# Kernel tuning notes

Measured on AMD Instinct MI355X. Metric: run time of the kernel, lower is better.

The kernel has to match this reference:

```python
import jax, jax.numpy as jnp
import numpy as np
from jax import lax

B, C_IN, T = 1024, 9, 2048
RT = T // 4            # reduced timesteps after two MaxPool(2)
HID, OUT = 128, 64
N_NODES = B * RT


def _chain_edges(rt, batch):
    """Bidirectional chain graph per sample, offset per batch element (PyG fallback)."""
    i = np.arange(rt - 1)
    src = np.concatenate([i, i + 1])   # edge_index[0] = source j
    dst = np.concatenate([i + 1, i])   # edge_index[1] = target i
    off = (np.arange(batch) * rt)[:, None]
    src = (src[None, :] + off).reshape(-1)
    dst = (dst[None, :] + off).reshape(-1)
    # degree with self-loops (GCNConv adds self-loops): endpoints 2, interior 3
    deg = np.full(rt, 3.0, np.float32)
    deg[0] = deg[-1] = 2.0
    deg = np.tile(deg, batch)
    return jnp.asarray(src, jnp.int32), jnp.asarray(dst, jnp.int32), jnp.asarray(deg ** -0.5)


def _conv1d(x, w, b):
    # x: [B, Cin, T], w: [Cout, Cin, 5] -> [B, Cout, T] (padding=2)
    y = lax.conv_general_dilated(x, w, window_strides=(1,), padding=[(2, 2)],
                                 dimension_numbers=('NCH', 'OIH', 'NCH'))
    return y + b[None, :, None]


def _maxpool2(x):
    b, c, t = x.shape
    return x.reshape(b, c, t // 2, 2).max(axis=-1)


def _gcn(x, W, b, src, dst, dinv):
    # GCNConv: x' = D^-1/2 (A+I) D^-1/2 (x W) + b
    h = x @ W                                        # [N, F]
    norm_e = (dinv[src] * dinv[dst])[:, None]        # per-edge sym norm
    agg = jax.ops.segment_sum(h[src] * norm_e, dst, num_segments=h.shape[0])
    return agg + h * (dinv * dinv)[:, None] + b      # self-loop term: 1/deg


def setup_inputs() -> dict:
    key = jax.random.key(0)
    ks = jax.random.split(key, 12)
    s = lambda k, shp, sc: jax.random.normal(k, shp, jnp.float32) * sc
    return {
        'x': jax.random.normal(ks[0], (B, C_IN, T), jnp.float32),
        'conv1_w': s(ks[1], (16, C_IN, 5), 0.15), 'conv1_b': jnp.zeros((16,), jnp.float32),
        'conv2_w': s(ks[2], (32, 16, 5), 0.1),   'conv2_b': jnp.zeros((32,), jnp.float32),
        'gcn1_w': s(ks[3], (32, HID), 0.17),     'gcn1_b': jnp.zeros((HID,), jnp.float32),
        'gcn2_w': s(ks[4], (HID, HID), 0.09),    'gcn2_b': jnp.zeros((HID,), jnp.float32),
        'fc_w': s(ks[5], (HID, OUT), 0.09),      'fc_b': jnp.zeros((OUT,), jnp.float32),
    }


def reference(x, conv1_w, conv1_b, conv2_w, conv2_b,
              gcn1_w, gcn1_b, gcn2_w, gcn2_b, fc_w, fc_b):
    b, c, t = x.shape
    h = _maxpool2(jax.nn.relu(_conv1d(x, conv1_w, conv1_b)))   # [B,16,T/2]
    h = _maxpool2(jax.nn.relu(_conv1d(h, conv2_w, conv2_b)))   # [B,32,T/4]
    rt = h.shape[-1]
    h = jnp.transpose(h, (0, 2, 1)).reshape(b * rt, 32)        # [N,32]
    src, dst, dinv = _chain_edges(rt, b)
    h = jax.nn.relu(_gcn(h, gcn1_w, gcn1_b, src, dst, dinv))
    h = jax.nn.relu(_gcn(h, gcn2_w, gcn2_b, src, dst, dinv))
    h = h.reshape(b, rt, -1).mean(axis=1)                      # [B,HID]
    return h @ fc_w + fc_b                                     # [B,OUT]
```

## Files before the change

### kernel.cpp

```cpp
#include <hip/hip_runtime.h>
#include <hip/hip_bf16.h>

#define B_      1024
#define CIN     9
#define T0_     2048
#define C1_     16
#define C2_     32
#define RT_     512
#define NNODES  (B_ * RT_)
#define HID_    128
#define OUTF_   64

typedef __attribute__((ext_vector_type(8))) __bf16 bf16x8;
typedef __attribute__((ext_vector_type(4))) float f32x4;
typedef __attribute__((ext_vector_type(8))) unsigned short us8;

__device__ __forceinline__ float bf2f(unsigned short u) {
    union { unsigned int i; float f; } c; c.i = ((unsigned int)u) << 16; return c.f;
}
__device__ __forceinline__ unsigned short f2bf1(float f) {
    union { float f; unsigned int i; } c; c.f = f;
    return (unsigned short)((c.i + 0x8000u) >> 16);
}
__device__ __forceinline__ unsigned int f2bf2(float lo, float hi) {
    union { float f; unsigned int i; } a, b; a.f = lo; b.f = hi;
    return __builtin_amdgcn_perm(b.i + 0x8000u, a.i + 0x8000u, 0x07060302u);
}
__device__ __forceinline__ float dinv_of(int r) {
    return (r == 0 || r == RT_ - 1) ? 0.70710678118f : 0.57735026919f;
}

__global__ __launch_bounds__(256) void repack_w(
    const float* __restrict__ W1g, const float* __restrict__ W2g,
    const float* __restrict__ Wc1g, const float* __restrict__ Wc2g,
    unsigned short* __restrict__ Wb1, unsigned short* __restrict__ Wb2,
    unsigned short* __restrict__ Wc1, unsigned short* __restrict__ Wc2)
{
    const int tid = threadIdx.x;
    const int bid = blockIdx.x;
    if (bid < 8) {
        for (int i = tid; i < 512; i += 256) {
            int s = bid * 512 + i;
            int k = s >> 7, f = s & 127;
            int lane = ((k >> 3) << 4) + (f & 15);
            int e = (((f >> 4) * 64) + lane) * 8 + (k & 7);
            Wb1[e] = f2bf1(W1g[s]);
        }
    } else if (bid < 24) {
        for (int i = tid; i < 1024; i += 256) {
            int s = (bid - 8) * 1024 + i;
            int k = s >> 7, f = s & 127;
            int ks = k >> 5, lane = (((k >> 3) & 3) << 4) + (f & 15);
            int e = ((ks * 8 + (f >> 4)) * 64 + lane) * 8 + (k & 7);
            Wb2[e] = f2bf1(W2g[s]);
        }
    } else if (bid < 28) {
        for (int i = tid; i < 384; i += 256) {
            int e = (bid - 24) * 384 + i;
            int j = e & 7, lane = (e >> 3) & 63, ks = e >> 9;
            int kk = ks * 32 + (lane >> 4) * 8 + j;
            int k = kk >> 4, ci = kk & 15, co = lane & 15;
            Wc1[e] = (k < 5 && ci < CIN) ? f2bf1(Wc1g[(co * CIN + ci) * 5 + k]) : 0;
        }
    } else {
        for (int i = tid; i < 768; i += 256) {
            int e = (bid - 28) * 768 + i;
            int j = e & 7, lane = (e >> 3) & 63, nt = (e >> 9) & 1, ks = e >> 10;
            int kk = ks * 32 + (lane >> 4) * 8 + j;
            int k = kk >> 4, ci = kk & 15, co = nt * 16 + (lane & 15);
            Wc2[e] = (k < 5) ? f2bf1(Wc2g[(co * C1_ + ci) * 5 + k]) : 0;
        }
    }
}

__global__ __launch_bounds__(256, 4) void mega(
    const float* __restrict__ x,
    const unsigned short* __restrict__ Wc1,
    const unsigned short* __restrict__ Wc2,
    const unsigned short* __restrict__ Wb1,
    const unsigned short* __restrict__ Wb2,
    const float* __restrict__ c1b, const float* __restrict__ c2b,
    const float* __restrict__ g1b, const float* __restrict__ g2b,
    float* __restrict__ partials)
{
    __shared__ __align__(16) unsigned char lds[40032];
    unsigned short* xs    = (unsigned short*)(lds);
    unsigned short* y1ext = (unsigned short*)(lds + 26496);
    unsigned short* y2loc = (unsigned short*)(lds);
    unsigned short* As1   = (unsigned short*)(lds + 10560);
    unsigned short* Hq    = (unsigned short*)(lds + 22080);
    unsigned short* A2q   = (unsigned short*)(lds + 31328);

    const int tid = threadIdx.x;
    const int b = blockIdx.x >> 2;
    const int r0 = (blockIdx.x & 3) * 128;

    const int lane = tid & 63, wave = tid >> 6;
    const int m = lane & 15, q = lane >> 4;
    const int ft0 = wave * 2;

    bf16x8 wfB[3];
    #pragma unroll
    for (int ks = 0; ks < 3; ks++) wfB[ks] = *(const bf16x8*)(Wc1 + (ks * 64 + lane) * 8);

    {
        const float* xb = x + (size_t)b * CIN * T0_;
        const int xbase = 4 * r0 - 14;
        for (int s = tid; s < 552; s += 256) {
            const int xt = xbase + s;
            union { us8 v; unsigned int u[4]; } o0, o1;
            if (xt >= 0 && xt < T0_) {
                float xv[9];
                #pragma unroll
                for (int ci = 0; ci < 9; ci++) xv[ci] = xb[ci * T0_ + xt];
                o0.u[0] = f2bf2(xv[0], xv[1]); o0.u[1] = f2bf2(xv[2], xv[3]);
                o0.u[2] = f2bf2(xv[4], xv[5]); o0.u[3] = f2bf2(xv[6], xv[7]);
                o1.u[0] = f2bf2(xv[8], 0.f);   o1.u[1] = o1.u[2] = o1.u[3] = 0;
            } else {
                o0.u[0] = o0.u[1] = o0.u[2] = o0.u[3] = 0;
                o1.u[0] = o1.u[1] = o1.u[2] = o1.u[3] = 0;
            }
            *(us8*)(xs + s * 24) = o0.v;
            *(us8*)(xs + s * 24 + 8) = o1.v;
        }
    }
    bf16x8 wfC[3][2];
    #pragma unroll
    for (int ks = 0; ks < 3; ks++)
        #pragma unroll
        for (int nt = 0; nt < 2; nt++)
            wfC[ks][nt] = *(const bf16x8*)(Wc2 + ((ks * 2 + nt) * 64 + lane) * 8);
    __syncthreads();

    {
        const float bv = c1b[m];
        const int t1base = 2 * r0 - 6;
        for (int mt = wave; mt < 34; mt += 4) {
            f32x4 acc = {};
            #pragma unroll
            for (int ks = 0; ks < 3; ks++) {
                const int row = mt * 16 + m + ks * 2 + (q >> 1);
                const bf16x8 af = *(const bf16x8*)(xs + row * 24 + (q & 1) * 8);
                acc = __builtin_amdgcn_mfma_f32_16x16x32_bf16(af, wfB[ks], acc, 0, 0, 0);
            }
            const int prow = mt * 8 + q * 2;
            const int t1a = t1base + prow, t1b = t1a + 1;
            const float p0 = fmaxf(fmaxf(acc[0], acc[1]) + bv, 0.f);
            const float p1 = fmaxf(fmaxf(acc[2], acc[3]) + bv, 0.f);
            if (prow < 268)
                y1ext[prow * 24 + m] = (t1a >= 0 && t1a < 1024) ? f2bf1(p0) : (unsigned short)0;
            if (prow + 1 < 268)
                y1ext[(prow + 1) * 24 + m] = (t1b >= 0 && t1b < 1024) ? f2bf1(p1) : (unsigned short)0;
        }
        for (int idx = tid; idx < 288; idx += 256) y1ext[268 * 24 + idx] = 0;
    }
    __syncthreads();

    {
        const float bv0 = c2b[m], bv1 = c2b[16 + m];
        for (int mt = wave; mt < 17; mt += 4) {
            f32x4 a0 = {}, a1 = {};
            #pragma unroll
            for (int ks = 0; ks < 3; ks++) {
                const int row = mt * 16 + m + ks * 2 + (q >> 1);
                const bf16x8 af = *(const bf16x8*)(y1ext + row * 24 + (q & 1) * 8);
                a0 = __builtin_amdgcn_mfma_f32_16x16x32_bf16(af, wfC[ks][0], a0, 0, 0, 0);
                a1 = __builtin_amdgcn_mfma_f32_16x16x32_bf16(af, wfC[ks][1], a1, 0, 0, 0);
            }
            const int nrow = mt * 8 + q * 2;
            if (nrow < 132) {
                y2loc[nrow * 40 + m]      = f2bf1(fmaxf(fmaxf(a0[0], a0[1]) + bv0, 0.f));
                y2loc[nrow * 40 + 16 + m] = f2bf1(fmaxf(fmaxf(a1[0], a1[1]) + bv1, 0.f));
            }
            if (nrow + 1 < 132) {
                y2loc[(nrow + 1) * 40 + m]      = f2bf1(fmaxf(fmaxf(a0[2], a0[3]) + bv0, 0.f));
                y2loc[(nrow + 1) * 40 + 16 + m] = f2bf1(fmaxf(fmaxf(a1[2], a1[3]) + bv1, 0.f));
            }
        }
    }
    bf16x8 wfE[2];
    wfE[0] = *(const bf16x8*)(Wb1 + (ft0 * 64 + lane) * 8);
    wfE[1] = *(const bf16x8*)(Wb1 + ((ft0 + 1) * 64 + lane) * 8);
    __syncthreads();

    for (int s = tid; s < 288; s += 256) {
        const int i = s >> 1, fh = (s & 1) * 16;
        unsigned short* dst = As1 + i * 40 + fh;
        const int r = r0 - 1 + i;
        union { us8 v; unsigned int u[4]; } o0, o1;
        if (i >= 130 || r < 0 || r >= RT_) {
            o0.u[0] = o0.u[1] = o0.u[2] = o0.u[3] = 0;
            o1.u[0] = o1.u[1] = o1.u[2] = o1.u[3] = 0;
        } else {
            const float dm = dinv_of(r), cm = dm * dm;
            const unsigned short* Yc = y2loc + (i + 1) * 40 + fh;
            us8 c0 = *(const us8*)(Yc), c1 = *(const us8*)(Yc + 8);
            float v[16];
            #pragma unroll
            for (int j = 0; j < 8; j++) { v[j] = cm * bf2f(c0[j]); v[8 + j] = cm * bf2f(c1[j]); }
            if (r > 0) {
                const float cl = dm * dinv_of(r - 1);
                us8 a0 = *(const us8*)(Yc - 40), a1 = *(const us8*)(Yc - 32);
                #pragma unroll
                for (int j = 0; j < 8; j++) { v[j] += cl * bf2f(a0[j]); v[8 + j] += cl * bf2f(a1[j]); }
            }
            if (r < RT_ - 1) {
                const float cr = dm * dinv_of(r + 1);
                us8 a0 = *(const us8*)(Yc + 40), a1 = *(const us8*)(Yc + 48);
                #pragma unroll
                for (int j = 0; j < 8; j++) { v[j] += cr * bf2f(a0[j]); v[8 + j] += cr * bf2f(a1[j]); }
            }
            #pragma unroll
            for (int i2 = 0; i2 < 4; i2++) {
                o0.u[i2] = f2bf2(v[2 * i2], v[2 * i2 + 1]);
                o1.u[i2] = f2bf2(v[8 + 2 * i2], v[9 + 2 * i2]);
            }
        }
        *(us8*)dst = o0.v; *(us8*)(dst + 8) = o1.v;
    }
    bf16x8 bw[4][2];
    #pragma unroll
    for (int ks = 0; ks < 4; ks++)
        #pragma unroll
        for (int i = 0; i < 2; i++)
            bw[ks][i] = *(const bf16x8*)(Wb2 + ((size_t)((ks * 8 + wave * 2 + i) * 64 + lane)) * 8);
    const float4 bv0 = *(const float4*)&g1b[ft0 * 16 + q * 4];
    const float4 bv1 = *(const float4*)&g1b[(ft0 + 1) * 16 + q * 4];
    const float bb0 = g2b[wave * 32 + m];
    const float bb1 = g2b[wave * 32 + 16 + m];
    __syncthreads();

    const f32x4 zz = {};

    auto do_E = [&](int qi) {
        #pragma unroll
        for (int nt = 0; nt < 3; nt++) {
            const bf16x8 bfr = *(const bf16x8*)(As1 + (qi * 32 + nt * 16 + m) * 40 + q * 8);
            f32x4 o0 = __builtin_amdgcn_mfma_f32_16x16x32_bf16(wfE[0], bfr, zz, 0, 0, 0);
            f32x4 o1 = __builtin_amdgcn_mfma_f32_16x16x32_bf16(wfE[1], bfr, zz, 0, 0, 0);
            const int hrow = nt * 16 + m;
            if (hrow < 34) {
                union { ushort4 s; unsigned int u[2]; } w0, w1;
                w0.u[0] = f2bf2(fmaxf(o0[0] + bv0.x, 0.f), fmaxf(o0[1] + bv0.y, 0.f));
                w0.u[1] = f2bf2(fmaxf(o0[2] + bv0.z, 0.f), fmaxf(o0[3] + bv0.w, 0.f));
                w1.u[0] = f2bf2(fmaxf(o1[0] + bv1.x, 0.f), fmaxf(o1[1] + bv1.y, 0.f));
                w1.u[1] = f2bf2(fmaxf(o1[2] + bv1.z, 0.f), fmaxf(o1[3] + bv1.w, 0.f));
                *(ushort4*)(Hq + hrow * 136 + ft0 * 16 + q * 4) = w0.s;
                *(ushort4*)(Hq + hrow * 136 + (ft0 + 1) * 16 + q * 4) = w1.s;
            }
        }
    };

    do_E(0);
    __syncthreads();

    float s0 = 0.f, s1 = 0.f;
    for (int qi = 0; qi < 4; qi++) {
        {
            const int jl = tid >> 3, fh = (tid & 7) * 16;
            const int r = r0 + qi * 32 + jl;
            const float dm = dinv_of(r), cm = dm * dm;
            const float cl = (r > 0) ? dm * dinv_of(r - 1) : 0.f;
            const float cr = (r < RT_ - 1) ? dm * dinv_of(r + 1) : 0.f;
            const unsigned short* Hl = Hq + jl * 136 + fh;
            const unsigned short* Hc = Hl + 136;
            const unsigned short* Hr = Hc + 136;
            unsigned short* dst = A2q + jl * 136 + fh;
            #pragma unroll
            for (int c = 0; c < 2; c++) {
                us8 cc = *(const us8*)(Hc + c * 8);
                us8 ll = *(const us8*)(Hl + c * 8);
                us8 rr = *(const us8*)(Hr + c * 8);
                float v[8];
                #pragma unroll
                for (int e = 0; e < 8; e++)
                    v[e] = cm * bf2f(cc[e]) + cl * bf2f(ll[e]) + cr * bf2f(rr[e]);
                union { us8 v; unsigned int u[4]; } o;
                #pragma unroll
                for (int i2 = 0; i2 < 4; i2++) o.u[i2] = f2bf2(v[2 * i2], v[2 * i2 + 1]);
                *(us8*)(dst + c * 8) = o.v;
            }
        }
        __syncthreads();

        {
            f32x4 acc2[2][2] = {};
            #pragma unroll
            for (int ntl = 0; ntl < 2; ntl++)
                #pragma unroll
                for (int ks = 0; ks < 4; ks++) {
                    const bf16x8 af = *(const bf16x8*)(A2q + (ntl * 16 + m) * 136 + ks * 32 + q * 8);
                    acc2[ntl][0] = __builtin_amdgcn_mfma_f32_16x16x32_bf16(af, bw[ks][0], acc2[ntl][0], 0, 0, 0);
                    acc2[ntl][1] = __builtin_amdgcn_mfma_f32_16x16x32_bf16(af, bw[ks][1], acc2[ntl][1], 0, 0, 0);
                }
            #pragma unroll
            for (int ntl = 0; ntl < 2; ntl++)
                #pragma unroll
                for (int rgi = 0; rgi < 4; rgi++) {
                    s0 += fmaxf(acc2[ntl][0][rgi] + bb0, 0.f);
                    s1 += fmaxf(acc2[ntl][1][rgi] + bb1, 0.f);
                }
        }
        if (qi < 3) {
            do_E(qi + 1);
            __syncthreads();
        }
    }

    {
        s0 += __shfl_xor(s0, 16, 64); s0 += __shfl_xor(s0, 32, 64);
        s1 += __shfl_xor(s1, 16, 64); s1 += __shfl_xor(s1, 32, 64);
        if (lane < 16) {
            float* p = partials + (size_t)blockIdx.x * 128 + wave * 32;
            p[m] = s0;
            p[16 + m] = s1;
        }
    }
}

__global__ __launch_bounds__(128) void fc_kernel(
    const float* __restrict__ partials, const float* __restrict__ fw,
    const float* __restrict__ fb, float* __restrict__ out)
{
    __shared__ float sm[128];
    const int b = blockIdx.x, tid = threadIdx.x;
    float s = 0.f;
    #pragma unroll
    for (int t = 0; t < 4; t++) s += partials[((b << 2) + t) * 128 + tid];
    sm[tid] = s * (1.0f / 512.0f);
    __syncthreads();
    if (tid < 64) {
        float acc = fb[tid];
        #pragma unroll 8
        for (int f = 0; f < 128; f++) acc += sm[f] * fw[f * 64 + tid];
        out[b * 64 + tid] = acc;
    }
}

extern "C" void kernel_launch(void* const* d_in, const int* in_sizes, int n_in,
                              void* d_out, int out_size, void* d_ws, size_t ws_size,
                              hipStream_t stream)
{
    const float* x   = (const float*)d_in[0];
    const float* w1  = (const float*)d_in[1];
    const float* b1  = (const float*)d_in[2];
    const float* w2  = (const float*)d_in[3];
    const float* b2  = (const float*)d_in[4];
    const float* g1w = (const float*)d_in[5];
    const float* g1b = (const float*)d_in[6];
    const float* g2w = (const float*)d_in[7];
    const float* g2b = (const float*)d_in[8];
    const float* fw  = (const float*)d_in[9];
    const float* fb  = (const float*)d_in[10];

    char* ws = (char*)d_ws;
    float* partials     = (float*)(ws);
    unsigned short* Wb1 = (unsigned short*)(ws + 2097152);
    unsigned short* Wb2 = (unsigned short*)(ws + 2097152 + 16384);
    unsigned short* Wc1 = (unsigned short*)(ws + 2097152 + 65536);
    unsigned short* Wc2 = (unsigned short*)(ws + 2097152 + 81920);
    float* out = (float*)d_out;

    repack_w<<<32, 256, 0, stream>>>(g1w, g2w, w1, w2, Wb1, Wb2, Wc1, Wc2);
    mega<<<NNODES / 128, 256, 0, stream>>>(x, Wc1, Wc2, Wb1, Wb2,
                                           b1, b2, g1b, g2b, partials);
    fc_kernel<<<B_, 128, 0, stream>>>(partials, fw, fb, out);
}
```

Measured before the change: 183.5 us.

## Reorder second GCN layer as transform-then-aggregate using register shuffles

```diff
diff --git a/kernel.cpp b/kernel.cpp
--- a/kernel.cpp
+++ b/kernel.cpp
@@ -83,13 +83,12 @@
     const float* __restrict__ g1b, const float* __restrict__ g2b,
     float* __restrict__ partials)
 {
-    __shared__ __align__(16) unsigned char lds[40032];
+    __shared__ __align__(16) unsigned char lds[39936];
     unsigned short* xs    = (unsigned short*)(lds);
     unsigned short* y1ext = (unsigned short*)(lds + 26496);
     unsigned short* y2loc = (unsigned short*)(lds);
     unsigned short* As1   = (unsigned short*)(lds + 10560);
     unsigned short* Hq    = (unsigned short*)(lds + 22080);
-    unsigned short* A2q   = (unsigned short*)(lds + 31328);
 
     const int tid = threadIdx.x;
     const int b = blockIdx.x >> 2;
@@ -239,7 +238,7 @@
             f32x4 o0 = __builtin_amdgcn_mfma_f32_16x16x32_bf16(wfE[0], bfr, zz, 0, 0, 0);
             f32x4 o1 = __builtin_amdgcn_mfma_f32_16x16x32_bf16(wfE[1], bfr, zz, 0, 0, 0);
             const int hrow = nt * 16 + m;
-            if (hrow < 34) {
+            if (nt < 2 || m < 2) {
                 union { ushort4 s; unsigned int u[2]; } w0, w1;
                 w0.u[0] = f2bf2(fmaxf(o0[0] + bv0.x, 0.f), fmaxf(o0[1] + bv0.y, 0.f));
                 w0.u[1] = f2bf2(fmaxf(o0[2] + bv0.z, 0.f), fmaxf(o0[3] + bv0.w, 0.f));
@@ -251,57 +250,83 @@
         }
     };
 
+    auto row_acc = [&](float prevv, float curv, float nextv, int r, bool edgeQ, float bias) -> float {
+        float cl, cm, cr;
+        if (edgeQ) {
+            if (r < 0 || r >= RT_) return 0.f;
+            const float dm = dinv_of(r);
+            cm = dm * dm;
+            cl = (r > 0) ? dm * dinv_of(r - 1) : 0.f;
+            cr = (r < RT_ - 1) ? dm * dinv_of(r + 1) : 0.f;
+        } else {
+            cl = cm = cr = (1.f / 3.f);
+        }
+        const float agg = cl * prevv + cm * curv + cr * nextv;
+        return fmaxf(agg + bias, 0.f);
+    };
+
+    float s0 = 0.f, s1 = 0.f;
+
+    auto do_Gp = [&](int qi) {
+        f32x4 Pa[3] = {}, Pb[3] = {};
+        #pragma unroll
+        for (int ks = 0; ks < 4; ks++) {
+            #pragma unroll
+            for (int nt = 0; nt < 3; nt++) {
+                const bf16x8 af = *(const bf16x8*)(Hq + (nt * 16 + m) * 136 + ks * 32 + q * 8);
+                Pa[nt] = __builtin_amdgcn_mfma_f32_16x16x32_bf16(af, bw[ks][0], Pa[nt], 0, 0, 0);
+                Pb[nt] = __builtin_amdgcn_mfma_f32_16x16x32_bf16(af, bw[ks][1], Pb[nt], 0, 0, 0);
+            }
+        }
+        const int rbase = r0 + qi * 32 - 1;
+        const bool edgeQ = (r0 == 0 && qi == 0) || (r0 == 384 && qi == 3);
+        #pragma unroll
+        for (int i = 0; i < 2; i++) {
+            const f32x4 p0 = i ? Pb[0] : Pa[0];
+            const f32x4 p1 = i ? Pb[1] : Pa[1];
+            const f32x4 p2 = i ? Pb[2] : Pa[2];
+            const float bias = i ? bb1 : bb0;
+            const float t0_up = __shfl(p0[0], (lane + 16) & 63);
+            const float t0_ux = __shfl(p1[0], (lane - 48) & 63);
+            const float t0_dn = __shfl(p0[3], (lane - 16) & 63);
+            const float t1_up = __shfl(p1[0], (lane + 16) & 63);
+            const float t1_ux = __shfl(p2[0], (lane - 48) & 63);
+            const float t1_dn = __shfl(p1[3], (lane - 16) & 63);
+            const float t1_dx = __shfl(p0[3], (lane + 48) & 63);
+            const float t2_dx = __shfl(p1[3], (lane + 48) & 63);
+            float ss = 0.f;
+            {
+                const float prev[4] = { (q > 0) ? t0_dn : 0.f, p0[0], p0[1], p0[2] };
+                const float next[4] = { p0[1], p0[2], p0[3], (q < 3) ? t0_up : t0_ux };
+                #pragma unroll
+                for (int g2 = 0; g2 < 4; g2++) {
+                    const float v = row_acc(prev[g2], p0[g2], next[g2],
+                                            rbase + q * 4 + g2, edgeQ, bias);
+                    ss += (q == 0 && g2 == 0) ? 0.f : v;
+                }
+            }
+            {
+                const float prev[4] = { (q > 0) ? t1_dn : t1_dx, p1[0], p1[1], p1[2] };
+                const float next[4] = { p1[1], p1[2], p1[3], (q < 3) ? t1_up : t1_ux };
+                #pragma unroll
+                for (int g2 = 0; g2 < 4; g2++)
+                    ss += row_acc(prev[g2], p1[g2], next[g2],
+                                  rbase + 16 + q * 4 + g2, edgeQ, bias);
+            }
+            {
+                const float v = row_acc(t2_dx, p2[0], p2[1], rbase + 32, edgeQ, bias);
+                ss += (q == 0) ? v : 0.f;
+            }
+            if (i == 0) s0 += ss; else s1 += ss;
+        }
+    };
+
     do_E(0);
     __syncthreads();
-
-    float s0 = 0.f, s1 = 0.f;
     for (int qi = 0; qi < 4; qi++) {
-        {
-            const int jl = tid >> 3, fh = (tid & 7) * 16;
-            const int r = r0 + qi * 32 + jl;
-            const float dm = dinv_of(r), cm = dm * dm;
-            const float cl = (r > 0) ? dm * dinv_of(r - 1) : 0.f;
-            const float cr = (r < RT_ - 1) ? dm * dinv_of(r + 1) : 0.f;
-            const unsigned short* Hl = Hq + jl * 136 + fh;
-            const unsigned short* Hc = Hl + 136;
-            const unsigned short* Hr = Hc + 136;
-            unsigned short* dst = A2q + jl * 136 + fh;
-            #pragma unroll
-            for (int c = 0; c < 2; c++) {
-                us8 cc = *(const us8*)(Hc + c * 8);
-                us8 ll = *(const us8*)(Hl + c * 8);
-                us8 rr = *(const us8*)(Hr + c * 8);
-                float v[8];
-                #pragma unroll
-                for (int e = 0; e < 8; e++)
-                    v[e] = cm * bf2f(cc[e]) + cl * bf2f(ll[e]) + cr * bf2f(rr[e]);
-                union { us8 v; unsigned int u[4]; } o;
-                #pragma unroll
-                for (int i2 = 0; i2 < 4; i2++) o.u[i2] = f2bf2(v[2 * i2], v[2 * i2 + 1]);
-                *(us8*)(dst + c * 8) = o.v;
-            }
-        }
-        __syncthreads();
-
-        {
-            f32x4 acc2[2][2] = {};
-            #pragma unroll
-            for (int ntl = 0; ntl < 2; ntl++)
-                #pragma unroll
-                for (int ks = 0; ks < 4; ks++) {
-                    const bf16x8 af = *(const bf16x8*)(A2q + (ntl * 16 + m) * 136 + ks * 32 + q * 8);
-                    acc2[ntl][0] = __builtin_amdgcn_mfma_f32_16x16x32_bf16(af, bw[ks][0], acc2[ntl][0], 0, 0, 0);
-                    acc2[ntl][1] = __builtin_amdgcn_mfma_f32_16x16x32_bf16(af, bw[ks][1], acc2[ntl][1], 0, 0, 0);
-                }
-            #pragma unroll
-            for (int ntl = 0; ntl < 2; ntl++)
-                #pragma unroll
-                for (int rgi = 0; rgi < 4; rgi++) {
-                    s0 += fmaxf(acc2[ntl][0][rgi] + bb0, 0.f);
-                    s1 += fmaxf(acc2[ntl][1][rgi] + bb1, 0.f);
-                }
-        }
+        do_Gp(qi);
         if (qi < 3) {
+            __syncthreads();
             do_E(qi + 1);
             __syncthreads();
         }
```

Result: slower. 211.3 us (+15.2%).

## Give each wave a private LDS arena and time slice to drop block barriers

Applied to the files above, without the earlier changes.

```diff
diff --git a/kernel.cpp b/kernel.cpp
--- a/kernel.cpp
+++ b/kernel.cpp
@@ -73,7 +73,7 @@
     }
 }
 
-__global__ __launch_bounds__(256, 4) void mega(
+__global__ __launch_bounds__(256, 3) void mega(
     const float* __restrict__ x,
     const unsigned short* __restrict__ Wc1,
     const unsigned short* __restrict__ Wc2,
@@ -83,21 +83,22 @@
     const float* __restrict__ g1b, const float* __restrict__ g2b,
     float* __restrict__ partials)
 {
-    __shared__ __align__(16) unsigned char lds[40032];
-    unsigned short* xs    = (unsigned short*)(lds);
-    unsigned short* y1ext = (unsigned short*)(lds + 26496);
-    unsigned short* y2loc = (unsigned short*)(lds);
-    unsigned short* As1   = (unsigned short*)(lds + 10560);
-    unsigned short* Hq    = (unsigned short*)(lds + 22080);
-    unsigned short* A2q   = (unsigned short*)(lds + 31328);
+    __shared__ __align__(16) unsigned char lds[53760];
 
     const int tid = threadIdx.x;
     const int b = blockIdx.x >> 2;
     const int r0 = (blockIdx.x & 3) * 128;
-
     const int lane = tid & 63, wave = tid >> 6;
     const int m = lane & 15, q = lane >> 4;
-    const int ft0 = wave * 2;
+    const int w32 = wave * 32;
+
+    unsigned short* arena = (unsigned short*)lds + wave * 6720;
+    unsigned short* xs  = arena;
+    unsigned short* y1  = arena + 4608;
+    unsigned short* y2  = arena + 2432;
+    unsigned short* As1 = arena;
+    unsigned short* Hq  = arena + 1920;
+    unsigned short* A2q = arena + 4368;
 
     bf16x8 wfB[3];
     #pragma unroll
@@ -105,8 +106,10 @@
 
     {
         const float* xb = x + (size_t)b * CIN * T0_;
-        const int xbase = 4 * r0 - 14;
-        for (int s = tid; s < 552; s += 256) {
+        const int xbase = 4 * r0 - 14 + 128 * wave;
+        #pragma unroll
+        for (int i = 0; i < 3; i++) {
+            const int s = lane + 64 * i;
             const int xt = xbase + s;
             union { us8 v; unsigned int u[4]; } o0, o1;
             if (xt >= 0 && xt < T0_) {
@@ -124,18 +127,11 @@
             *(us8*)(xs + s * 24 + 8) = o1.v;
         }
     }
-    bf16x8 wfC[3][2];
-    #pragma unroll
-    for (int ks = 0; ks < 3; ks++)
-        #pragma unroll
-        for (int nt = 0; nt < 2; nt++)
-            wfC[ks][nt] = *(const bf16x8*)(Wc2 + ((ks * 2 + nt) * 64 + lane) * 8);
-    __syncthreads();
 
     {
         const float bv = c1b[m];
-        const int t1base = 2 * r0 - 6;
-        for (int mt = wave; mt < 34; mt += 4) {
+        const int t1base = 2 * r0 - 6 + 64 * wave;
+        for (int mt = 0; mt < 11; mt++) {
             f32x4 acc = {};
             #pragma unroll
             for (int ks = 0; ks < 3; ks++) {
@@ -147,68 +143,66 @@
             const int t1a = t1base + prow, t1b = t1a + 1;
             const float p0 = fmaxf(fmaxf(acc[0], acc[1]) + bv, 0.f);
             const float p1 = fmaxf(fmaxf(acc[2], acc[3]) + bv, 0.f);
-            if (prow < 268)
-                y1ext[prow * 24 + m] = (t1a >= 0 && t1a < 1024) ? f2bf1(p0) : (unsigned short)0;
-            if (prow + 1 < 268)
-                y1ext[(prow + 1) * 24 + m] = (t1b >= 0 && t1b < 1024) ? f2bf1(p1) : (unsigned short)0;
-        }
-        for (int idx = tid; idx < 288; idx += 256) y1ext[268 * 24 + idx] = 0;
-    }
-    __syncthreads();
+            y1[prow * 24 + m]       = (t1a >= 0 && t1a < 1024) ? f2bf1(p0) : (unsigned short)0;
+            y1[(prow + 1) * 24 + m] = (t1b >= 0 && t1b < 1024) ? f2bf1(p1) : (unsigned short)0;
+        }
+    }
 
     {
+        bf16x8 wfC[3][2];
+        #pragma unroll
+        for (int ks = 0; ks < 3; ks++)
+            #pragma unroll
+            for (int nt = 0; nt < 2; nt++)
+                wfC[ks][nt] = *(const bf16x8*)(Wc2 + ((ks * 2 + nt) * 64 + lane) * 8);
         const float bv0 = c2b[m], bv1 = c2b[16 + m];
-        for (int mt = wave; mt < 17; mt += 4) {
+        for (int mt = 0; mt < 5; mt++) {
             f32x4 a0 = {}, a1 = {};
             #pragma unroll
             for (int ks = 0; ks < 3; ks++) {
                 const int row = mt * 16 + m + ks * 2 + (q >> 1);
-                const bf16x8 af = *(const bf16x8*)(y1ext + row * 24 + (q & 1) * 8);
+                const bf16x8 af = *(const bf16x8*)(y1 + row * 24 + (q & 1) * 8);
                 a0 = __builtin_amdgcn_mfma_f32_16x16x32_bf16(af, wfC[ks][0], a0, 0, 0, 0);
                 a1 = __builtin_amdgcn_mfma_f32_16x16x32_bf16(af, wfC[ks][1], a1, 0, 0, 0);
             }
             const int nrow = mt * 8 + q * 2;
-            if (nrow < 132) {
-                y2loc[nrow * 40 + m]      = f2bf1(fmaxf(fmaxf(a0[0], a0[1]) + bv0, 0.f));
-                y2loc[nrow * 40 + 16 + m] = f2bf1(fmaxf(fmaxf(a1[0], a1[1]) + bv1, 0.f));
-            }
-            if (nrow + 1 < 132) {
-                y2loc[(nrow + 1) * 40 + m]      = f2bf1(fmaxf(fmaxf(a0[2], a0[3]) + bv0, 0.f));
-                y2loc[(nrow + 1) * 40 + 16 + m] = f2bf1(fmaxf(fmaxf(a1[2], a1[3]) + bv1, 0.f));
-            }
-        }
-    }
-    bf16x8 wfE[2];
-    wfE[0] = *(const bf16x8*)(Wb1 + (ft0 * 64 + lane) * 8);
-    wfE[1] = *(const bf16x8*)(Wb1 + ((ft0 + 1) * 64 + lane) * 8);
-    __syncthreads();
-
-    for (int s = tid; s < 288; s += 256) {
-        const int i = s >> 1, fh = (s & 1) * 16;
-        unsigned short* dst = As1 + i * 40 + fh;
-        const int r = r0 - 1 + i;
+            if (nrow < 36) {
+                y2[nrow * 40 + m]      = f2bf1(fmaxf(fmaxf(a0[0], a0[1]) + bv0, 0.f));
+                y2[nrow * 40 + 16 + m] = f2bf1(fmaxf(fmaxf(a1[0], a1[1]) + bv1, 0.f));
+            }
+            if (nrow + 1 < 36) {
+                y2[(nrow + 1) * 40 + m]      = f2bf1(fmaxf(fmaxf(a0[2], a0[3]) + bv0, 0.f));
+                y2[(nrow + 1) * 40 + 16 + m] = f2bf1(fmaxf(fmaxf(a1[2], a1[3]) + bv1, 0.f));
+            }
+        }
+    }
+
+    for (int s2 = lane; s2 < 68; s2 += 64) {
+        const int j = s2 >> 1, fh = (s2 & 1) * 16;
+        unsigned short* dst = As1 + j * 40 + fh;
+        const int r = r0 + w32 - 1 + j;
         union { us8 v; unsigned int u[4]; } o0, o1;
-        if (i >= 130 || r < 0 || r >= RT_) {
+        if (r < 0 || r >= RT_) {
             o0.u[0] = o0.u[1] = o0.u[2] = o0.u[3] = 0;
             o1.u[0] = o1.u[1] = o1.u[2] = o1.u[3] = 0;
         } else {
             const float dm = dinv_of(r), cm = dm * dm;
-            const unsigned short* Yc = y2loc + (i + 1) * 40 + fh;
+            const unsigned short* Yc = y2 + (j + 1) * 40 + fh;
             us8 c0 = *(const us8*)(Yc), c1 = *(const us8*)(Yc + 8);
             float v[16];
             #pragma unroll
-            for (int j = 0; j < 8; j++) { v[j] = cm * bf2f(c0[j]); v[8 + j] = cm * bf2f(c1[j]); }
+            for (int jj = 0; jj < 8; jj++) { v[jj] = cm * bf2f(c0[jj]); v[8 + jj] = cm * bf2f(c1[jj]); }
             if (r > 0) {
                 const float cl = dm * dinv_of(r - 1);
                 us8 a0 = *(const us8*)(Yc - 40), a1 = *(const us8*)(Yc - 32);
                 #pragma unroll
-                for (int j = 0; j < 8; j++) { v[j] += cl * bf2f(a0[j]); v[8 + j] += cl * bf2f(a1[j]); }
+                for (int jj = 0; jj < 8; jj++) { v[jj] += cl * bf2f(a0[jj]); v[8 + jj] += cl * bf2f(a1[jj]); }
             }
             if (r < RT_ - 1) {
                 const float cr = dm * dinv_of(r + 1);
                 us8 a0 = *(const us8*)(Yc + 40), a1 = *(const us8*)(Yc + 48);
                 #pragma unroll
-                for (int j = 0; j < 8; j++) { v[j] += cr * bf2f(a0[j]); v[8 + j] += cr * bf2f(a1[j]); }
+                for (int jj = 0; jj < 8; jj++) { v[jj] += cr * bf2f(a0[jj]); v[8 + jj] += cr * bf2f(a1[jj]); }
             }
             #pragma unroll
             for (int i2 = 0; i2 < 4; i2++) {
@@ -218,47 +212,39 @@
         }
         *(us8*)dst = o0.v; *(us8*)(dst + 8) = o1.v;
     }
-    bf16x8 bw[4][2];
+
+    float bias_j[8];
     #pragma unroll
-    for (int ks = 0; ks < 4; ks++)
-        #pragma unroll
-        for (int i = 0; i < 2; i++)
-            bw[ks][i] = *(const bf16x8*)(Wb2 + ((size_t)((ks * 8 + wave * 2 + i) * 64 + lane)) * 8);
-    const float4 bv0 = *(const float4*)&g1b[ft0 * 16 + q * 4];
-    const float4 bv1 = *(const float4*)&g1b[(ft0 + 1) * 16 + q * 4];
-    const float bb0 = g2b[wave * 32 + m];
-    const float bb1 = g2b[wave * 32 + 16 + m];
-    __syncthreads();
+    for (int j = 0; j < 8; j++) bias_j[j] = g2b[j * 16 + m];
+    float s_acc[8] = {0.f, 0.f, 0.f, 0.f, 0.f, 0.f, 0.f, 0.f};
 
     const f32x4 zz = {};
 
-    auto do_E = [&](int qi) {
-        #pragma unroll
-        for (int nt = 0; nt < 3; nt++) {
-            const bf16x8 bfr = *(const bf16x8*)(As1 + (qi * 32 + nt * 16 + m) * 40 + q * 8);
-            f32x4 o0 = __builtin_amdgcn_mfma_f32_16x16x32_bf16(wfE[0], bfr, zz, 0, 0, 0);
-            f32x4 o1 = __builtin_amdgcn_mfma_f32_16x16x32_bf16(wfE[1], bfr, zz, 0, 0, 0);
-            const int hrow = nt * 16 + m;
-            if (hrow < 34) {
-                union { ushort4 s; unsigned int u[2]; } w0, w1;
-                w0.u[0] = f2bf2(fmaxf(o0[0] + bv0.x, 0.f), fmaxf(o0[1] + bv0.y, 0.f));
-                w0.u[1] = f2bf2(fmaxf(o0[2] + bv0.z, 0.f), fmaxf(o0[3] + bv0.w, 0.f));
-                w1.u[0] = f2bf2(fmaxf(o1[0] + bv1.x, 0.f), fmaxf(o1[1] + bv1.y, 0.f));
-                w1.u[1] = f2bf2(fmaxf(o1[2] + bv1.z, 0.f), fmaxf(o1[3] + bv1.w, 0.f));
-                *(ushort4*)(Hq + hrow * 136 + ft0 * 16 + q * 4) = w0.s;
-                *(ushort4*)(Hq + hrow * 136 + (ft0 + 1) * 16 + q * 4) = w1.s;
-            }
-        }
-    };
-
-    do_E(0);
-    __syncthreads();
-
-    float s0 = 0.f, s1 = 0.f;
-    for (int qi = 0; qi < 4; qi++) {
-        {
-            const int jl = tid >> 3, fh = (tid & 7) * 16;
-            const int r = r0 + qi * 32 + jl;
+    #pragma unroll 1
+    for (int hs = 0; hs < 2; hs++) {
+        #pragma unroll 2
+        for (int ft = 0; ft < 8; ft++) {
+            const bf16x8 wf = *(const bf16x8*)(Wb1 + ((size_t)(ft * 64 + lane)) * 8);
+            const float4 bvf = *(const float4*)&g1b[ft * 16 + q * 4];
+            #pragma unroll
+            for (int nt = 0; nt < 2; nt++) {
+                const bf16x8 bfr = *(const bf16x8*)(As1 + (hs * 16 + nt * 16 + m) * 40 + q * 8);
+                f32x4 o = __builtin_amdgcn_mfma_f32_16x16x32_bf16(wf, bfr, zz, 0, 0, 0);
+                const int hrow = nt * 16 + m;
+                if (hrow < 18) {
+                    union { ushort4 s; unsigned int u[2]; } w0;
+                    w0.u[0] = f2bf2(fmaxf(o[0] + bvf.x, 0.f), fmaxf(o[1] + bvf.y, 0.f));
+                    w0.u[1] = f2bf2(fmaxf(o[2] + bvf.z, 0.f), fmaxf(o[3] + bvf.w, 0.f));
+                    *(ushort4*)(Hq + hrow * 136 + ft * 16 + q * 4) = w0.s;
+                }
+            }
+        }
+
+        #pragma unroll
+        for (int u = 0; u < 2; u++) {
+            const int idx = lane + 64 * u;
+            const int jl = idx >> 3, fh = (idx & 7) * 16;
+            const int r = r0 + w32 + hs * 16 + jl;
             const float dm = dinv_of(r), cm = dm * dm;
             const float cl = (r > 0) ? dm * dinv_of(r - 1) : 0.f;
             const float cr = (r < RT_ - 1) ? dm * dinv_of(r + 1) : 0.f;
@@ -281,40 +267,44 @@
                 *(us8*)(dst + c * 8) = o.v;
             }
         }
-        __syncthreads();
 
         {
-            f32x4 acc2[2][2] = {};
-            #pragma unroll
-            for (int ntl = 0; ntl < 2; ntl++)
+            bf16x8 ga[4];
+            #pragma unroll
+            for (int ks = 0; ks < 4; ks++)
+                ga[ks] = *(const bf16x8*)(A2q + m * 136 + ks * 32 + q * 8);
+            #pragma unroll
+            for (int j = 0; j < 8; j++) {
+                f32x4 P = {};
                 #pragma unroll
                 for (int ks = 0; ks < 4; ks++) {
-                    const bf16x8 af = *(const bf16x8*)(A2q + (ntl * 16 + m) * 136 + ks * 32 + q * 8);
-                    acc2[ntl][0] = __builtin_amdgcn_mfma_f32_16x16x32_bf16(af, bw[ks][0], acc2[ntl][0], 0, 0, 0);
-                    acc2[ntl][1] = __builtin_amdgcn_mfma_f32_16x16x32_bf16(af, bw[ks][1], acc2[ntl][1], 0, 0, 0);
+                    const bf16x8 bwf = *(const bf16x8*)(Wb2 + ((size_t)((ks * 8 + j) * 64 + lane)) * 8);
+                    P = __builtin_amdgcn_mfma_f32_16x16x32_bf16(ga[ks], bwf, P, 0, 0, 0);
                 }
-            #pragma unroll
-            for (int ntl = 0; ntl < 2; ntl++)
-                #pragma unroll
-                for (int rgi = 0; rgi < 4; rgi++) {
-                    s0 += fmaxf(acc2[ntl][0][rgi] + bb0, 0.f);
-                    s1 += fmaxf(acc2[ntl][1][rgi] + bb1, 0.f);
-                }
-        }
-        if (qi < 3) {
-            do_E(qi + 1);
-            __syncthreads();
+                #pragma unroll
+                for (int rg = 0; rg < 4; rg++)
+                    s_acc[j] += fmaxf(P[rg] + bias_j[j], 0.f);
+            }
         }
     }
 
     {
-        s0 += __shfl_xor(s0, 16, 64); s0 += __shfl_xor(s0, 32, 64);
-        s1 += __shfl_xor(s1, 16, 64); s1 += __shfl_xor(s1, 32, 64);
-        if (lane < 16) {
-            float* p = partials + (size_t)blockIdx.x * 128 + wave * 32;
-            p[m] = s0;
-            p[16 + m] = s1;
-        }
+        float* scratch = (float*)(arena + 4608);
+        #pragma unroll
+        for (int j = 0; j < 8; j++) {
+            float v = s_acc[j];
+            v += __shfl_xor(v, 16, 64);
+            v += __shfl_xor(v, 32, 64);
+            if (lane < 16) scratch[j * 16 + m] = v;
+        }
+    }
+    __syncthreads();
+    if (tid < 128) {
+        float t = 0.f;
+        #pragma unroll
+        for (int w = 0; w < 4; w++)
+            t += ((const float*)((unsigned short*)lds + w * 6720 + 4608))[tid];
+        partials[(size_t)blockIdx.x * 128 + tid] = t;
     }
 }
 
```

Measured after the change: 253.8 us. 38.3% more time.
